# Kernel optimization log

Hardware: AMD Instinct MI355X
Metric: run time of the kernel (lower is better)

## Reference

```python
import jax, jax.numpy as jnp
import numpy as np

VOCAB = 8192
DIM = 256
COMMITMENT = 0.25


def setup_inputs() -> dict:
    key = jax.random.key(0)
    kx, ke = jax.random.split(key)
    x = jax.random.normal(kx, (8, 4096, DIM), dtype=jnp.float32)
    # torch init: uniform(-1/vocab_size, 1/vocab_size)
    emb = jax.random.uniform(ke, (VOCAB, DIM), dtype=jnp.float32,
                             minval=-1.0 / VOCAB, maxval=1.0 / VOCAB)
    return {"x": x, "emb": emb}


def reference(x, emb):
    x2 = jnp.sum(x * x, axis=-1, keepdims=True)          # [B, N, 1]
    e2 = jnp.sum(emb * emb, axis=-1)                      # [V]
    d2 = x2 + e2 - 2.0 * jnp.einsum('bnd,vd->bnv', x, emb)  # [B, N, V]
    idx = jnp.argmin(d2, axis=-1)                         # [B, N]
    quantised = emb[idx]                                  # [B, N, D]

    codebook_loss = jnp.mean((quantised - jax.lax.stop_gradient(x)) ** 2)
    e_latent_loss = jnp.mean((jax.lax.stop_gradient(quantised) - x) ** 2)
    loss = codebook_loss + COMMITMENT * e_latent_loss

    quantised_st = x + jax.lax.stop_gradient(quantised - x)  # straight-through
    return quantised_st, loss, codebook_loss, idx
```

## Files before the change

kernel.cpp:

```cpp
#include <hip/hip_runtime.h>

#define VOCAB 8192
#define DIM   256
#define NTOK  32768

#define LOSS_OFF 8388608
#define CB_OFF   8388609
#define IDX_OFF  8388610

#define X2_F     0
#define E2_F     32768
#define ACC_F    40960
#define OVF_I    40961
#define BEST_B   196608
#define EMB16_B  458752
#define SMAX_B   4718592
#define SCNT_B   38273024
#define BIN_B    38404096
#define CAP_S    8192
#define PSUM_B   46792704
#define WS_NEED  (PSUM_B + 8192 * 4)

#define M2 1.5e-4f
#define LCAP 16000

typedef __attribute__((ext_vector_type(8)))  short bf16x8;
typedef __attribute__((ext_vector_type(16))) float f32x16;

__global__ __launch_bounds__(256) void k_sums(const float* __restrict__ x,
                                              const float* __restrict__ emb,
                                              float* __restrict__ ws,
                                              unsigned long long* __restrict__ best,
                                              int* __restrict__ scnt,
                                              unsigned* __restrict__ e16u,
                                              int full) {
    const int lane = threadIdx.x & 63;
    const int wave = threadIdx.x >> 6;
    const int row  = blockIdx.x * 16 + wave * 4 + (lane >> 4);
    const int sub  = lane & 15;
    const int k    = sub & 7;
    const int half = sub >> 3;
    const float* src = (row < NTOK ? x + (size_t)row * DIM
                                   : emb + (size_t)(row - NTOK) * DIM)
                       + half * 128 + k;
    float r;
    {
        float v0 = src[0];
        float t0 = v0 * v0;
        asm volatile("" : "+v"(t0));
        r = t0;
        for (int i = 1; i < 16; ++i) {
            float w = src[8 * i];
            float u = w * w;
            asm volatile("" : "+v"(u));
            r = r + u;
        }
    }
    float t;
    t = __shfl_xor(r, 1, 64); r = r + t;
    t = __shfl_xor(r, 2, 64); r = r + t;
    t = __shfl_xor(r, 4, 64); r = r + t;
    t = __shfl_xor(r, 8, 64); r = r + t;
    if (sub == 0) ws[row] = r;

    if (full && row >= NTOK) {
        const int c = row - NTOK;
        const float* er = emb + (size_t)c * DIM + sub * 16;
        const float4 f0 = *(const float4*)(er + 0);
        const float4 f1 = *(const float4*)(er + 4);
        const float4 f2 = *(const float4*)(er + 8);
        const float4 f3 = *(const float4*)(er + 12);
        uint4 u0, u1;
        u0.x = (__float_as_uint(f0.y) & 0xFFFF0000u) | (__float_as_uint(f0.x) >> 16);
        u0.y = (__float_as_uint(f0.w) & 0xFFFF0000u) | (__float_as_uint(f0.z) >> 16);
        u0.z = (__float_as_uint(f1.y) & 0xFFFF0000u) | (__float_as_uint(f1.x) >> 16);
        u0.w = (__float_as_uint(f1.w) & 0xFFFF0000u) | (__float_as_uint(f1.z) >> 16);
        u1.x = (__float_as_uint(f2.y) & 0xFFFF0000u) | (__float_as_uint(f2.x) >> 16);
        u1.y = (__float_as_uint(f2.w) & 0xFFFF0000u) | (__float_as_uint(f2.z) >> 16);
        u1.z = (__float_as_uint(f3.y) & 0xFFFF0000u) | (__float_as_uint(f3.x) >> 16);
        u1.w = (__float_as_uint(f3.w) & 0xFFFF0000u) | (__float_as_uint(f3.z) >> 16);
        unsigned* dst = e16u + (((size_t)(c >> 5) * 16384 + (size_t)sub * 1024
                               + (size_t)(c & 31) * 16) >> 2);
        *(uint4*)dst         = u0;
        *(uint4*)(dst + 128) = u1;
    }

    const int gid = blockIdx.x * 256 + threadIdx.x;
    if (gid == 0) {
        ws[ACC_F] = 0.0f;
        ((int*)ws)[OVF_I] = 0;
    }
    if (full) {
        if (gid < NTOK) best[gid] = ~0ULL;
        if (gid < 256)  scnt[gid] = 0;
    }
}

__device__ __forceinline__ unsigned f_ord(float v) {
    unsigned u = __float_as_uint(v);
    return u ^ ((unsigned)((int)u >> 31) | 0x80000000u);
}
__device__ __forceinline__ float f_unord(unsigned k) {
    unsigned m = (k >> 31) ? 0x80000000u : 0xFFFFFFFFu;
    return __uint_as_float(k ^ m);
}

__global__ __launch_bounds__(512, 2) void k_coarse(
        const float* __restrict__ x, const unsigned short* __restrict__ embh,
        float* __restrict__ smax,
        unsigned* __restrict__ binned, int* __restrict__ scnt,
        int* __restrict__ ovf) {
    __shared__ unsigned tmax[128];
    __shared__ float tthr[128];
    __shared__ unsigned lbuf[2 + LCAP];
    __shared__ unsigned lcnt[256], lbase[256], lcur[256];

    const int tid  = threadIdx.x;
    const int lane = tid & 63, wid = tid >> 6;
    const int g = wid & 1, csub = wid >> 1;
    const int t_wave = blockIdx.x * 128 + g * 64;

    bf16x8 bx[2][16];
    {
        const int tok0 = t_wave + (lane & 31);
#pragma unroll
        for (int grp = 0; grp < 2; ++grp) {
            const float* xr = x + (size_t)(tok0 + grp * 32) * DIM + (lane >> 5) * 8;
#pragma unroll
            for (int kt = 0; kt < 16; ++kt) {
                float4 f0 = *(const float4*)(xr + kt * 16);
                float4 f1 = *(const float4*)(xr + kt * 16 + 4);
                union { bf16x8 v; unsigned u[4]; } P;
                P.u[0] = (__float_as_uint(f0.y) & 0xFFFF0000u) | (__float_as_uint(f0.x) >> 16);
                P.u[1] = (__float_as_uint(f0.w) & 0xFFFF0000u) | (__float_as_uint(f0.z) >> 16);
                P.u[2] = (__float_as_uint(f1.y) & 0xFFFF0000u) | (__float_as_uint(f1.x) >> 16);
                P.u[3] = (__float_as_uint(f1.w) & 0xFFFF0000u) | (__float_as_uint(f1.z) >> 16);
                bx[grp][kt] = P.v;
            }
        }
    }

    const char* ep = (const char*)embh + (size_t)csub * 16384 + (size_t)lane * 16;

    bf16x8 afA[8], afB[8];
#pragma unroll
    for (int j = 0; j < 8; ++j)
        afA[j] = *(const bf16x8*)(ep + j * 1024);

    float rmax = -3.0e38f;
    for (int n = 0; n < 64; ++n) {
        const char* epB = ep + 8192;
#pragma unroll
        for (int j = 0; j < 8; ++j)
            afB[j] = *(const bf16x8*)(epB + j * 1024);

        f32x16 acc0, acc1;
#pragma unroll
        for (int q = 0; q < 16; ++q) { acc0[q] = 0.0f; acc1[q] = 0.0f; }

        __builtin_amdgcn_s_setprio(1);
#pragma unroll
        for (int j = 0; j < 8; ++j) {
            acc0 = __builtin_amdgcn_mfma_f32_32x32x16_bf16(afA[j], bx[0][j], acc0, 0, 0, 0);
            acc1 = __builtin_amdgcn_mfma_f32_32x32x16_bf16(afA[j], bx[1][j], acc1, 0, 0, 0);
        }
        __builtin_amdgcn_s_setprio(0);

        const char* epn = ep + 65536;
        if (n < 63) {
#pragma unroll
            for (int j = 0; j < 8; ++j)
                afA[j] = *(const bf16x8*)(epn + j * 1024);
        }

        __builtin_amdgcn_s_setprio(1);
#pragma unroll
        for (int j = 0; j < 8; ++j) {
            acc0 = __builtin_amdgcn_mfma_f32_32x32x16_bf16(afB[j], bx[0][8 + j], acc0, 0, 0, 0);
            acc1 = __builtin_amdgcn_mfma_f32_32x32x16_bf16(afB[j], bx[1][8 + j], acc1, 0, 0, 0);
        }
        __builtin_amdgcn_s_setprio(0);
        ep = epn;

        float m0, m1;
        {
            float a = fmaxf(fmaxf(acc0[0], acc0[1]),  fmaxf(acc0[2], acc0[3]));
            float b = fmaxf(fmaxf(acc0[4], acc0[5]),  fmaxf(acc0[6], acc0[7]));
            float c = fmaxf(fmaxf(acc0[8], acc0[9]),  fmaxf(acc0[10], acc0[11]));
            float d = fmaxf(fmaxf(acc0[12], acc0[13]),fmaxf(acc0[14], acc0[15]));
            m0 = fmaxf(fmaxf(a, b), fmaxf(c, d));
            a = fmaxf(fmaxf(acc1[0], acc1[1]),  fmaxf(acc1[2], acc1[3]));
            b = fmaxf(fmaxf(acc1[4], acc1[5]),  fmaxf(acc1[6], acc1[7]));
            c = fmaxf(fmaxf(acc1[8], acc1[9]),  fmaxf(acc1[10], acc1[11]));
            d = fmaxf(fmaxf(acc1[12], acc1[13]),fmaxf(acc1[14], acc1[15]));
            m1 = fmaxf(fmaxf(a, b), fmaxf(c, d));
        }
        m0 = fmaxf(m0, __shfl_xor(m0, 32, 64));
        m1 = fmaxf(m1, __shfl_xor(m1, 32, 64));
        const float mv = (lane < 32) ? m0 : m1;
        rmax = fmaxf(rmax, mv);
        smax[(size_t)(n * 4 + csub) * NTOK + t_wave + lane] = mv;
    }

    if (tid < 128) tmax[tid] = 0u;
    if (tid == 0) lbuf[0] = 0u;
    if (tid < 256) { lcnt[tid] = 0u; lcur[tid] = 0u; }
    __syncthreads();
    atomicMax(&tmax[g * 64 + lane], f_ord(rmax));
    __syncthreads();
    if (tid < 128) tthr[tid] = f_unord(tmax[tid]) - M2;
    __syncthreads();

    const int t0b = blockIdx.x * 128;
    for (int r = 0; r < 64; ++r) {
        const int cell  = r * 512 + tid;
        const int stile = cell >> 7, tl = cell & 127;
        const float v = smax[(size_t)stile * NTOK + t0b + tl];
        if (v >= tthr[tl]) {
            const unsigned p = atomicAdd(&lbuf[0], 1u);
            if (p < LCAP)
                lbuf[2 + p] = ((unsigned)(t0b + tl) << 8) | (unsigned)stile;
        }
    }
    __syncthreads();
    unsigned bc = lbuf[0];
    if (bc > LCAP) { bc = LCAP; if (tid == 0) *ovf = 1; }

    for (unsigned i = tid; i < bc; i += 512)
        atomicAdd(&lcnt[lbuf[2 + i] & 255u], 1u);
    __syncthreads();
    if (tid < 256 && lcnt[tid]) {
        const unsigned b = (unsigned)atomicAdd(&scnt[tid], (int)lcnt[tid]);
        lbase[tid] = b;
        if (b + lcnt[tid] > CAP_S) *ovf = 1;
    }
    __syncthreads();
    for (unsigned i = tid; i < bc; i += 512) {
        const unsigned e = lbuf[2 + i];
        const unsigned s = e & 255u;
        const unsigned p = lbase[s] + atomicAdd(&lcur[s], 1u);
        if (p < CAP_S) binned[(size_t)s * CAP_S + p] = e;
    }
}

__device__ __forceinline__ float exact_score(const float* __restrict__ xr,
                                             const float* __restrict__ er,
                                             float x2t, float e2v) {
    float dot = 0.0f;
#pragma unroll 16
    for (int d = 0; d < DIM; d += 4) {
        const float4 e4 = *(const float4*)(er + d);
        const float4 x4 = *(const float4*)(xr + d);
        dot = fmaf(e4.x, x4.x, dot);
        dot = fmaf(e4.y, x4.y, dot);
        dot = fmaf(e4.z, x4.z, dot);
        dot = fmaf(e4.w, x4.w, dot);
    }
    const float A = x2t + e2v;
    return A - 2.0f * dot;
}

__global__ __launch_bounds__(256) void k_exact2(
        const float* __restrict__ x, const float* __restrict__ emb,
        const float* __restrict__ x2, const float* __restrict__ e2,
        const unsigned* __restrict__ binned, const int* __restrict__ scnt,
        const int* __restrict__ ovf, unsigned long long* __restrict__ best) {
    __shared__ float elds[32][257];
    __shared__ float e2s[32];
    const int s = blockIdx.x >> 3, sub = blockIdx.x & 7;
    {
        const int r = threadIdx.x >> 3, c0 = (threadIdx.x & 7) * 32;
        const float* er = emb + (size_t)(s * 32 + r) * DIM + c0;
#pragma unroll
        for (int q = 0; q < 8; ++q) {
            const float4 f = *(const float4*)(er + q * 4);
            elds[r][c0 + q * 4 + 0] = f.x; elds[r][c0 + q * 4 + 1] = f.y;
            elds[r][c0 + q * 4 + 2] = f.z; elds[r][c0 + q * 4 + 3] = f.w;
        }
        if (threadIdx.x < 32) e2s[threadIdx.x] = e2[s * 32 + threadIdx.x];
    }
    __syncthreads();

    const int lane = threadIdx.x & 63, wave = threadIdx.x >> 6;
    const int l5 = lane & 31, half = lane >> 5;
    int count = scnt[s]; if (count > CAP_S) count = CAP_S;
    const unsigned* bucket = binned + (size_t)s * CAP_S;
    const float e2v = e2s[l5];

    for (int k = (sub * 4 + wave) * 2 + half; k < count; k += 64) {
        const unsigned e = bucket[k];
        const int token  = (int)(e >> 8);
        const float* xr  = x + (size_t)token * DIM;
        const float x2t  = x2[token];
        float dot = 0.0f;
#pragma unroll 16
        for (int d = 0; d < DIM; d += 4) {
            const float4 x4 = *(const float4*)(xr + d);
            dot = fmaf(elds[l5][d + 0], x4.x, dot);
            dot = fmaf(elds[l5][d + 1], x4.y, dot);
            dot = fmaf(elds[l5][d + 2], x4.z, dot);
            dot = fmaf(elds[l5][d + 3], x4.w, dot);
        }
        const float A  = x2t + e2v;
        const float sc = A - 2.0f * dot;
        unsigned long long pk =
            ((unsigned long long)__float_as_uint(sc) << 32) | (unsigned)(s * 32 + l5);
#pragma unroll
        for (int m = 1; m < 32; m <<= 1) {
            unsigned long long o = __shfl_xor(pk, m, 64);
            if (o < pk) pk = o;
        }
        if (l5 == 0) atomicMin(&best[token], pk);
    }

    if (*ovf) {
        const size_t stride = (size_t)2048 * 256;
        for (size_t c = blockIdx.x * 256 + threadIdx.x;
             c < (size_t)NTOK * VOCAB; c += stride) {
            const int token = (int)(c >> 13);
            const int v     = (int)(c & (VOCAB - 1));
            const float sc = exact_score(x + (size_t)token * DIM, emb + (size_t)v * DIM,
                                         x2[token], e2[v]);
            unsigned long long pk =
                ((unsigned long long)__float_as_uint(sc) << 32) | (unsigned)v;
            atomicMin(&best[token], pk);
        }
    }
}

__global__ __launch_bounds__(512) void k_main_fb(
        const float* __restrict__ x, const float* __restrict__ emb,
        const float* __restrict__ x2, const float* __restrict__ e2,
        float* __restrict__ idxf) {
    __shared__ float xT[32][132];
    __shared__ float eT[32][260];
    const int tid = threadIdx.x;
    const int tx = tid & 31, ty = tid >> 5;
    const int t0 = blockIdx.x * 128;
    float x2r[8];
#pragma unroll
    for (int ii = 0; ii < 8; ++ii)
        x2r[ii] = x2[t0 + ((ii & 4) << 4) + ty * 4 + (ii & 3)];
    float tb[8]; int ti[8];
#pragma unroll
    for (int s = 0; s < 8; ++s) { tb[s] = 3.0e38f; ti[s] = 0; }
    const int xt = tid & 127, xc = tid >> 7;
    const int ev = tid & 255, ec0 = tid >> 8;
    for (int v0 = 0; v0 < VOCAB; v0 += 256) {
        float a[8][8];
#pragma unroll
        for (int i = 0; i < 8; ++i)
#pragma unroll
            for (int j = 0; j < 8; ++j) a[i][j] = 0.0f;
        for (int kk = 0; kk < DIM; kk += 32) {
            __syncthreads();
#pragma unroll
            for (int h = 0; h < 2; ++h) {
                const int kc = h * 16 + xc * 4;
                const float4 vx = *(const float4*)&x[(size_t)(t0 + xt) * DIM + kk + kc];
                xT[kc + 0][xt] = vx.x; xT[kc + 1][xt] = vx.y;
                xT[kc + 2][xt] = vx.z; xT[kc + 3][xt] = vx.w;
            }
#pragma unroll
            for (int h = 0; h < 4; ++h) {
                const int kc = (ec0 + 2 * h) * 4;
                const float4 ve = *(const float4*)&emb[(size_t)(v0 + ev) * DIM + kk + kc];
                eT[kc + 0][ev] = ve.x; eT[kc + 1][ev] = ve.y;
                eT[kc + 2][ev] = ve.z; eT[kc + 3][ev] = ve.w;
            }
            __syncthreads();
#pragma unroll 4
            for (int k = 0; k < 32; ++k) {
                float xa[8], eb[8];
                *(float4*)&xa[0] = *(const float4*)&xT[k][ty * 4];
                *(float4*)&xa[4] = *(const float4*)&xT[k][64 + ty * 4];
                *(float4*)&eb[0] = *(const float4*)&eT[k][tx * 4];
                *(float4*)&eb[4] = *(const float4*)&eT[k][128 + tx * 4];
#pragma unroll
                for (int i = 0; i < 8; ++i)
#pragma unroll
                    for (int j = 0; j < 8; ++j)
                        a[i][j] = fmaf(xa[i], eb[j], a[i][j]);
            }
        }
#pragma unroll
        for (int jj = 0; jj < 8; ++jj) {
            const int v = v0 + ((jj & 4) << 5) + tx * 4 + (jj & 3);
            const float evv = e2[v];
#pragma unroll
            for (int ii = 0; ii < 8; ++ii) {
                const float A  = x2r[ii] + evv;
                const float sc = A - 2.0f * a[ii][jj];
                if (sc < tb[ii]) { tb[ii] = sc; ti[ii] = v; }
            }
        }
    }
#pragma unroll
    for (int ii = 0; ii < 8; ++ii) {
        float b = tb[ii]; int bi = ti[ii];
#pragma unroll
        for (int m = 1; m < 32; m <<= 1) {
            const float ob = __shfl_xor(b, m, 64);
            const int   oi = __shfl_xor(bi, m, 64);
            if (ob < b || (ob == b && oi < bi)) { b = ob; bi = oi; }
        }
        if (tx == 0) {
            const int token = t0 + ((ii & 4) << 4) + ty * 4 + (ii & 3);
            idxf[token] = (float)bi;
        }
    }
}

__global__ __launch_bounds__(256) void k_gather(
        const float* __restrict__ x, const float* __restrict__ emb,
        const unsigned long long* __restrict__ best,
        float* __restrict__ out, float* __restrict__ psum,
        float* __restrict__ acc, int full) {
    const int token = blockIdx.x * 4 + (threadIdx.x >> 6);
    const int lane  = threadIdx.x & 63;
    float* idxf = out + IDX_OFF;
    int v;
    if (full) {
        v = (int)(unsigned)(best[token] & 0xFFFFFFFFULL);
        if (lane == 0) idxf[token] = (float)v;
    } else {
        v = (int)idxf[token];
    }
    const float4 e4 = *(const float4*)&emb[(size_t)v * DIM + lane * 4];
    const float4 x4 = *(const float4*)&x[(size_t)token * DIM + lane * 4];
    *(float4*)&out[(size_t)token * DIM + lane * 4] = e4;
    const float dx = e4.x - x4.x, dy = e4.y - x4.y, dz = e4.z - x4.z, dw = e4.w - x4.w;
    float s = dx*dx + dy*dy + dz*dz + dw*dw;
#pragma unroll
    for (int m = 1; m < 64; m <<= 1) s += __shfl_xor(s, m, 64);
    __shared__ float wsum[4];
    if (lane == 0) wsum[threadIdx.x >> 6] = s;
    __syncthreads();
    if (threadIdx.x == 0) {
        const float bsum = wsum[0] + wsum[1] + wsum[2] + wsum[3];
        if (full) psum[blockIdx.x] = bsum;
        else      atomicAdd(acc, bsum);
    }
}

__global__ __launch_bounds__(256) void k_final(const float* __restrict__ psum,
                                               const float* __restrict__ acc,
                                               float* __restrict__ out, int full) {
    float s = 0.0f;
    if (full) {
        for (int i = threadIdx.x; i < 8192; i += 256) s += psum[i];
#pragma unroll
        for (int m = 1; m < 64; m <<= 1) s += __shfl_xor(s, m, 64);
        __shared__ float wsum[4];
        if ((threadIdx.x & 63) == 0) wsum[threadIdx.x >> 6] = s;
        __syncthreads();
        s = wsum[0] + wsum[1] + wsum[2] + wsum[3];
    } else {
        s = *acc;
    }
    if (threadIdx.x == 0) {
        const float cb = s * (1.0f / 8388608.0f);
        out[LOSS_OFF] = 1.25f * cb;
        out[CB_OFF]   = cb;
    }
}

extern "C" void kernel_launch(void* const* d_in, const int* in_sizes, int n_in,
                              void* d_out, int out_size, void* d_ws, size_t ws_size,
                              hipStream_t stream) {
    const float* x   = (const float*)d_in[0];
    const float* emb = (const float*)d_in[1];
    float* out  = (float*)d_out;
    char*  wsB  = (char*)d_ws;
    float* wsF  = (float*)d_ws;

    float* x2   = wsF + X2_F;
    float* e2   = wsF + E2_F;
    float* acc  = wsF + ACC_F;
    int*   ovf  = (int*)wsF + OVF_I;
    unsigned long long* best = (unsigned long long*)(wsB + BEST_B);
    unsigned short*     e16  = (unsigned short*)(wsB + EMB16_B);
    float*              smax = (float*)(wsB + SMAX_B);
    int*                scnt = (int*)(wsB + SCNT_B);
    unsigned*           binned = (unsigned*)(wsB + BIN_B);
    float*              psum = (float*)(wsB + PSUM_B);
    float* idxf = out + IDX_OFF;

    const int full = (ws_size >= (size_t)WS_NEED) ? 1 : 0;

    k_sums<<<(NTOK + VOCAB) / 16, 256, 0, stream>>>(x, emb, wsF, best, scnt,
                                                    (unsigned*)e16, full);
    if (full) {
        k_coarse<<<256, 512, 0, stream>>>(x, e16, smax, binned, scnt, ovf);
        k_exact2<<<2048, 256, 0, stream>>>(x, emb, x2, e2, binned, scnt, ovf, best);
    } else {
        k_main_fb<<<NTOK / 128, 512, 0, stream>>>(x, emb, x2, e2, idxf);
    }
    k_gather<<<NTOK / 4, 256, 0, stream>>>(x, emb, best, out, psum, acc, full);
    k_final <<<1, 256, 0, stream>>>(psum, acc, out, full);
}
```

Before: 283.9 us.

## Split MFMA accumulators, batch gather tokens per block, shrink candidate list cap

The coarse MFMA loop now alternates between two independent accumulator pairs and sums them before the max reduction, breaking the serial dependency chain through each accumulator. The gather kernel processes four tokens per wave across 2048 blocks instead of one token per wave across 8192 blocks, so k_final reduces fewer partial sums. LCAP is lowered from 16000 to 4096, which changes the local candidate buffer limit and may trigger overflow handling more often. The extra accumulators add register pressure.

Result: slower. 297.5 us (+4.8%).

```diff
diff --git a/kernel.cpp b/kernel.cpp
--- a/kernel.cpp
+++ b/kernel.cpp
@@ -22,7 +22,7 @@
 #define WS_NEED  (PSUM_B + 8192 * 4)
 
 #define M2 1.5e-4f
-#define LCAP 16000
+#define LCAP 4096
 
 typedef __attribute__((ext_vector_type(8)))  short bf16x8;
 typedef __attribute__((ext_vector_type(16))) float f32x16;
@@ -154,15 +154,19 @@
         for (int j = 0; j < 8; ++j)
             afB[j] = *(const bf16x8*)(epB + j * 1024);
 
-        f32x16 acc0, acc1;
-#pragma unroll
-        for (int q = 0; q < 16; ++q) { acc0[q] = 0.0f; acc1[q] = 0.0f; }
+        f32x16 acc0a, acc0b, acc1a, acc1b;
+#pragma unroll
+        for (int q = 0; q < 16; ++q) {
+            acc0a[q] = 0.0f; acc0b[q] = 0.0f; acc1a[q] = 0.0f; acc1b[q] = 0.0f;
+        }
 
         __builtin_amdgcn_s_setprio(1);
 #pragma unroll
-        for (int j = 0; j < 8; ++j) {
-            acc0 = __builtin_amdgcn_mfma_f32_32x32x16_bf16(afA[j], bx[0][j], acc0, 0, 0, 0);
-            acc1 = __builtin_amdgcn_mfma_f32_32x32x16_bf16(afA[j], bx[1][j], acc1, 0, 0, 0);
+        for (int j = 0; j < 8; j += 2) {
+            acc0a = __builtin_amdgcn_mfma_f32_32x32x16_bf16(afA[j],     bx[0][j],     acc0a, 0, 0, 0);
+            acc1a = __builtin_amdgcn_mfma_f32_32x32x16_bf16(afA[j],     bx[1][j],     acc1a, 0, 0, 0);
+            acc0b = __builtin_amdgcn_mfma_f32_32x32x16_bf16(afA[j + 1], bx[0][j + 1], acc0b, 0, 0, 0);
+            acc1b = __builtin_amdgcn_mfma_f32_32x32x16_bf16(afA[j + 1], bx[1][j + 1], acc1b, 0, 0, 0);
         }
         __builtin_amdgcn_s_setprio(0);
 
@@ -175,24 +179,42 @@
 
         __builtin_amdgcn_s_setprio(1);
 #pragma unroll
-        for (int j = 0; j < 8; ++j) {
-            acc0 = __builtin_amdgcn_mfma_f32_32x32x16_bf16(afB[j], bx[0][8 + j], acc0, 0, 0, 0);
-            acc1 = __builtin_amdgcn_mfma_f32_32x32x16_bf16(afB[j], bx[1][8 + j], acc1, 0, 0, 0);
+        for (int j = 0; j < 8; j += 2) {
+            acc0a = __builtin_amdgcn_mfma_f32_32x32x16_bf16(afB[j],     bx[0][8 + j],     acc0a, 0, 0, 0);
+            acc1a = __builtin_amdgcn_mfma_f32_32x32x16_bf16(afB[j],     bx[1][8 + j],     acc1a, 0, 0, 0);
+            acc0b = __builtin_amdgcn_mfma_f32_32x32x16_bf16(afB[j + 1], bx[0][8 + j + 1], acc0b, 0, 0, 0);
+            acc1b = __builtin_amdgcn_mfma_f32_32x32x16_bf16(afB[j + 1], bx[1][8 + j + 1], acc1b, 0, 0, 0);
         }
         __builtin_amdgcn_s_setprio(0);
         ep = epn;
 
         float m0, m1;
         {
-            float a = fmaxf(fmaxf(acc0[0], acc0[1]),  fmaxf(acc0[2], acc0[3]));
-            float b = fmaxf(fmaxf(acc0[4], acc0[5]),  fmaxf(acc0[6], acc0[7]));
-            float c = fmaxf(fmaxf(acc0[8], acc0[9]),  fmaxf(acc0[10], acc0[11]));
-            float d = fmaxf(fmaxf(acc0[12], acc0[13]),fmaxf(acc0[14], acc0[15]));
+            float s0 = acc0a[0] + acc0b[0],  s1 = acc0a[1] + acc0b[1];
+            float s2 = acc0a[2] + acc0b[2],  s3 = acc0a[3] + acc0b[3];
+            float s4 = acc0a[4] + acc0b[4],  s5 = acc0a[5] + acc0b[5];
+            float s6 = acc0a[6] + acc0b[6],  s7 = acc0a[7] + acc0b[7];
+            float s8 = acc0a[8] + acc0b[8],  s9 = acc0a[9] + acc0b[9];
+            float sA = acc0a[10] + acc0b[10], sB = acc0a[11] + acc0b[11];
+            float sC = acc0a[12] + acc0b[12], sD = acc0a[13] + acc0b[13];
+            float sE = acc0a[14] + acc0b[14], sF = acc0a[15] + acc0b[15];
+            float a = fmaxf(fmaxf(s0, s1), fmaxf(s2, s3));
+            float b = fmaxf(fmaxf(s4, s5), fmaxf(s6, s7));
+            float c = fmaxf(fmaxf(s8, s9), fmaxf(sA, sB));
+            float d = fmaxf(fmaxf(sC, sD), fmaxf(sE, sF));
             m0 = fmaxf(fmaxf(a, b), fmaxf(c, d));
-            a = fmaxf(fmaxf(acc1[0], acc1[1]),  fmaxf(acc1[2], acc1[3]));
-            b = fmaxf(fmaxf(acc1[4], acc1[5]),  fmaxf(acc1[6], acc1[7]));
-            c = fmaxf(fmaxf(acc1[8], acc1[9]),  fmaxf(acc1[10], acc1[11]));
-            d = fmaxf(fmaxf(acc1[12], acc1[13]),fmaxf(acc1[14], acc1[15]));
+            s0 = acc1a[0] + acc1b[0];  s1 = acc1a[1] + acc1b[1];
+            s2 = acc1a[2] + acc1b[2];  s3 = acc1a[3] + acc1b[3];
+            s4 = acc1a[4] + acc1b[4];  s5 = acc1a[5] + acc1b[5];
+            s6 = acc1a[6] + acc1b[6];  s7 = acc1a[7] + acc1b[7];
+            s8 = acc1a[8] + acc1b[8];  s9 = acc1a[9] + acc1b[9];
+            sA = acc1a[10] + acc1b[10]; sB = acc1a[11] + acc1b[11];
+            sC = acc1a[12] + acc1b[12]; sD = acc1a[13] + acc1b[13];
+            sE = acc1a[14] + acc1b[14]; sF = acc1a[15] + acc1b[15];
+            a = fmaxf(fmaxf(s0, s1), fmaxf(s2, s3));
+            b = fmaxf(fmaxf(s4, s5), fmaxf(s6, s7));
+            c = fmaxf(fmaxf(s8, s9), fmaxf(sA, sB));
+            d = fmaxf(fmaxf(sC, sD), fmaxf(sE, sF));
             m1 = fmaxf(fmaxf(a, b), fmaxf(c, d));
         }
         m0 = fmaxf(m0, __shfl_xor(m0, 32, 64));
@@ -416,30 +438,35 @@
         const unsigned long long* __restrict__ best,
         float* __restrict__ out, float* __restrict__ psum,
         float* __restrict__ acc, int full) {
-    const int token = blockIdx.x * 4 + (threadIdx.x >> 6);
-    const int lane  = threadIdx.x & 63;
+    const int lane = threadIdx.x & 63;
     float* idxf = out + IDX_OFF;
-    int v;
-    if (full) {
-        v = (int)(unsigned)(best[token] & 0xFFFFFFFFULL);
-        if (lane == 0) idxf[token] = (float)v;
-    } else {
-        v = (int)idxf[token];
-    }
-    const float4 e4 = *(const float4*)&emb[(size_t)v * DIM + lane * 4];
-    const float4 x4 = *(const float4*)&x[(size_t)token * DIM + lane * 4];
-    *(float4*)&out[(size_t)token * DIM + lane * 4] = e4;
-    const float dx = e4.x - x4.x, dy = e4.y - x4.y, dz = e4.z - x4.z, dw = e4.w - x4.w;
-    float s = dx*dx + dy*dy + dz*dz + dw*dw;
-#pragma unroll
-    for (int m = 1; m < 64; m <<= 1) s += __shfl_xor(s, m, 64);
+    float bsum = 0.0f;
+#pragma unroll
+    for (int it = 0; it < 4; ++it) {
+        const int token = (it * 2048 + blockIdx.x) * 4 + (threadIdx.x >> 6);
+        int v;
+        if (full) {
+            v = (int)(unsigned)(best[token] & 0xFFFFFFFFULL);
+            if (lane == 0) idxf[token] = (float)v;
+        } else {
+            v = (int)idxf[token];
+        }
+        const float4 e4 = *(const float4*)&emb[(size_t)v * DIM + lane * 4];
+        const float4 x4 = *(const float4*)&x[(size_t)token * DIM + lane * 4];
+        *(float4*)&out[(size_t)token * DIM + lane * 4] = e4;
+        const float dx = e4.x - x4.x, dy = e4.y - x4.y;
+        const float dz = e4.z - x4.z, dw = e4.w - x4.w;
+        bsum += dx*dx + dy*dy + dz*dz + dw*dw;
+    }
+#pragma unroll
+    for (int m = 1; m < 64; m <<= 1) bsum += __shfl_xor(bsum, m, 64);
     __shared__ float wsum[4];
-    if (lane == 0) wsum[threadIdx.x >> 6] = s;
+    if (lane == 0) wsum[threadIdx.x >> 6] = bsum;
     __syncthreads();
     if (threadIdx.x == 0) {
-        const float bsum = wsum[0] + wsum[1] + wsum[2] + wsum[3];
-        if (full) psum[blockIdx.x] = bsum;
-        else      atomicAdd(acc, bsum);
+        const float s = wsum[0] + wsum[1] + wsum[2] + wsum[3];
+        if (full) psum[blockIdx.x] = s;
+        else      atomicAdd(acc, s);
     }
 }
 
@@ -448,7 +475,7 @@
                                                float* __restrict__ out, int full) {
     float s = 0.0f;
     if (full) {
-        for (int i = threadIdx.x; i < 8192; i += 256) s += psum[i];
+        for (int i = threadIdx.x; i < 2048; i += 256) s += psum[i];
 #pragma unroll
         for (int m = 1; m < 64; m <<= 1) s += __shfl_xor(s, m, 64);
         __shared__ float wsum[4];
@@ -496,6 +523,6 @@
     } else {
         k_main_fb<<<NTOK / 128, 512, 0, stream>>>(x, emb, x2, e2, idxf);
     }
-    k_gather<<<NTOK / 4, 256, 0, stream>>>(x, emb, best, out, psum, acc, full);
+    k_gather<<<2048, 256, 0, stream>>>(x, emb, best, out, psum, acc, full);
     k_final <<<1, 256, 0, stream>>>(psum, acc, out, full);
 }
```
